# Kernel optimization log

Measured on AMD Instinct MI355X. Metric: run time of the kernel, lower is better.

## Reference

```python
import jax, jax.numpy as jnp
import numpy as np

ALPHA = 1.0  # DPMConfig.alpha
N, D, K = 4096, 256, 64


def setup_inputs() -> dict:
    key = jax.random.key(0)
    k1, k2, k3, k4 = jax.random.split(key, 4)
    x = jax.random.normal(k1, (N, D), dtype=jnp.float32)
    means = jax.random.normal(k2, (K, D), dtype=jnp.float32)
    # SPD covariances: A A^T / D + 0.5 I
    A = jax.random.normal(k3, (K, D, D), dtype=jnp.float32)
    covs = jnp.einsum('kde,kfe->kdf', A, A) / D + 0.5 * jnp.eye(D, dtype=jnp.float32)
    counts = jax.random.uniform(k4, (K,), dtype=jnp.float32, minval=1.0, maxval=200.0)
    n_points = 100000
    return {"x": x, "means": means, "covs": covs, "counts": counts, "n_points": n_points}


def reference(x, means, covs, counts, n_points):
    n, d = x.shape
    k = means.shape[0]
    # deviations from every cluster mean: [N, K, D]
    dev = x[:, None, :] - means[None, :, :]
    # batched Mahalanobis solve: covs broadcast over points
    solved = jnp.linalg.solve(covs[None], dev[..., None])[..., 0]  # [N, K, D]
    quad = jnp.sum(dev * solved, axis=-1)  # [N, K]
    # logdet with the same jitter as the original
    _, log_dets = jnp.linalg.slogdet(covs + 1e-10 * jnp.eye(d, dtype=covs.dtype))  # [K]
    log_lik = -0.5 * (d * jnp.log(2.0 * jnp.pi) + log_dets[None, :] + quad)  # [N, K]
    denom = jnp.asarray(n_points, jnp.float32) + ALPHA
    log_prior = jnp.log(counts / denom)  # [K]
    log_new = jnp.log(ALPHA / denom)
    log_probs = jnp.concatenate(
        [log_lik + log_prior[None, :], jnp.full((n, 1), log_new, dtype=x.dtype)], axis=1
    )  # [N, K+1]
    # stable normalize (max-subtract + exp + sum == softmax)
    probs = jax.nn.softmax(log_probs, axis=1)
    return probs
```

## Files before the change

### kernel.cpp

```cpp
#include <hip/hip_runtime.h>
#include <math.h>


#define DD 256
#define KC 64
#define NPTS 4096
#define NT 64
#define BB 64
#define KG 8
#define CH 4
#define NCH (DD / CH)

__global__ __launch_bounds__(512) void pivot_kernel(
    const float* __restrict__ covs, float* __restrict__ S,
    float* __restrict__ Plbuf, float* __restrict__ ldp, int bs)
{
  const int k = blockIdx.x;
  const int by = blockIdx.y;
  const int tid = threadIdx.x;
  float* Pb = Plbuf + (size_t)k * BB * BB;

  __shared__ __align__(16) float Tl[BB][BB + 4];
  __shared__ __align__(16) float pivc[2][BB];
  __shared__ __align__(16) float pivr[2][BB];

  if (by < 4) {
    if (bs == 0) return;
    const int j0p = (bs - 1) * BB;
    const int r0 = by * BB;
    const float* src = ((bs == 1) ? covs : (const float*)S) + (size_t)k * DD * DD;
    float* dst = S + (size_t)k * DD * DD;

    const int rr = tid >> 3;
    const int cc = (tid & 7) * 8;
    *reinterpret_cast<float4*>(&Tl[rr][cc]) =
        *reinterpret_cast<const float4*>(&Pb[rr * BB + cc]);
    *reinterpret_cast<float4*>(&Tl[rr][cc + 4]) =
        *reinterpret_cast<const float4*>(&Pb[rr * BB + cc + 4]);
    __syncthreads();

    const int r = r0 + rr;
    if (r0 == j0p) {
      *reinterpret_cast<float4*>(&dst[(size_t)r * DD + j0p + cc]) =
          *reinterpret_cast<const float4*>(&Tl[rr][cc]);
      *reinterpret_cast<float4*>(&dst[(size_t)r * DD + j0p + cc + 4]) =
          *reinterpret_cast<const float4*>(&Tl[rr][cc + 4]);
    } else {
      float Crow[BB];
      #pragma unroll
      for (int p = 0; p < BB; p += 4) {
        float4 cv = *reinterpret_cast<const float4*>(&src[(size_t)r * DD + j0p + p]);
        Crow[p] = cv.x; Crow[p + 1] = cv.y; Crow[p + 2] = cv.z; Crow[p + 3] = cv.w;
      }
      float acc[8] = {0.f, 0.f, 0.f, 0.f, 0.f, 0.f, 0.f, 0.f};
      #pragma unroll
      for (int p = 0; p < BB; ++p) {
        float4 t0 = *reinterpret_cast<const float4*>(&Tl[p][cc]);
        float4 t1 = *reinterpret_cast<const float4*>(&Tl[p][cc + 4]);
        acc[0] = fmaf(Crow[p], t0.x, acc[0]);
        acc[1] = fmaf(Crow[p], t0.y, acc[1]);
        acc[2] = fmaf(Crow[p], t0.z, acc[2]);
        acc[3] = fmaf(Crow[p], t0.w, acc[3]);
        acc[4] = fmaf(Crow[p], t1.x, acc[4]);
        acc[5] = fmaf(Crow[p], t1.y, acc[5]);
        acc[6] = fmaf(Crow[p], t1.z, acc[6]);
        acc[7] = fmaf(Crow[p], t1.w, acc[7]);
      }
      float4 o0 = {-acc[0], -acc[1], -acc[2], -acc[3]};
      float4 o1 = {-acc[4], -acc[5], -acc[6], -acc[7]};
      *reinterpret_cast<float4*>(&dst[(size_t)r * DD + j0p + cc]) = o0;
      *reinterpret_cast<float4*>(&dst[(size_t)r * DD + j0p + cc + 4]) = o1;
    }
    return;
  }

  if (bs == 4) return;

  const int j0 = bs * BB;
  const float* psrc = ((bs == 0) ? covs : (const float*)S) + (size_t)k * DD * DD;
  const int pr = tid >> 3;
  const int pc = (tid & 7) * 8;

  float v[8];
  {
    float4 a4 = *reinterpret_cast<const float4*>(&psrc[(size_t)(j0 + pr) * DD + j0 + pc]);
    float4 b4 = *reinterpret_cast<const float4*>(&psrc[(size_t)(j0 + pr) * DD + j0 + pc + 4]);
    v[0] = a4.x; v[1] = a4.y; v[2] = a4.z; v[3] = a4.w;
    v[4] = b4.x; v[5] = b4.y; v[6] = b4.z; v[7] = b4.w;
  }
  if (pc == 0) pivc[0][pr] = v[0];
  if (pr == 0) {
    #pragma unroll
    for (int e = 0; e < 8; ++e) pivr[0][pc + e] = v[e];
  }
  __syncthreads();

  float ld = 0.0f;
  #pragma unroll 1
  for (int p = 0; p < BB; ++p) {
    const int cur = p & 1, nxt = cur ^ 1;
    const float d = pivc[cur][p];
    const float inv_d = 1.0f / d;
    if (tid == 0) ld += logf(d);
    const float cr = pivc[cur][pr];
    float rw[8];
    *reinterpret_cast<float4*>(&rw[0]) = *reinterpret_cast<const float4*>(&pivr[cur][pc]);
    *reinterpret_cast<float4*>(&rw[4]) = *reinterpret_cast<const float4*>(&pivr[cur][pc + 4]);
    #pragma unroll
    for (int e = 0; e < 8; ++e) {
      float ge = fmaf(-inv_d * cr, rw[e], v[e]);
      if (pr == p)     ge = rw[e] * inv_d;
      if (pc + e == p) ge = (pr == p) ? -inv_d : cr * inv_d;
      v[e] = ge;
    }
    if (p < BB - 1) {
      if (pr == p + 1) {
        #pragma unroll
        for (int e = 0; e < 8; ++e) pivr[nxt][pc + e] = v[e];
      }
      if (pc <= p + 1 && p + 1 < pc + 8) pivc[nxt][pr] = v[p + 1 - pc];
    }
    __syncthreads();
  }

  float4 s0 = {v[0], v[1], v[2], v[3]};
  float4 s1 = {v[4], v[5], v[6], v[7]};
  *reinterpret_cast<float4*>(&Pb[pr * BB + pc]) = s0;
  *reinterpret_cast<float4*>(&Pb[pr * BB + pc + 4]) = s1;
  if (tid == 0) ldp[bs * KC + k] = ld;
}

__global__ __launch_bounds__(512) void update_kernel(
    const float* __restrict__ covs, float* __restrict__ S,
    const float* __restrict__ Plbuf, int bs)
{
  const int k = blockIdx.x;
  const int si = blockIdx.y;
  const int t = si + (si >= bs ? 1 : 0);
  const int c0 = t * BB;
  const int j0 = bs * BB;
  const int tid = threadIdx.x;
  const float* src = ((bs == 0) ? covs : (const float*)S) + (size_t)k * DD * DD;
  float* dst = S + (size_t)k * DD * DD;

  __shared__ __align__(16) float Pl[BB][BB + 4];
  __shared__ __align__(16) float SJ[BB][BB + 4];
  __shared__ __align__(16) float Tl[BB][BB + 4];

  const float* Pb = Plbuf + (size_t)k * BB * BB;
  #pragma unroll
  for (int q = 0; q < 8; ++q) {
    int e = q * 512 + tid;
    int r = e >> 6, c = e & 63;
    Pl[r][c] = Pb[e];
    SJ[r][c] = src[(size_t)(j0 + r) * DD + c0 + c];
  }
  __syncthreads();

  {
    const int c = tid & 63;
    const int rg = (tid >> 6) * 8;
    float tv[8];
    #pragma unroll
    for (int r = 0; r < 8; ++r) tv[r] = 0.0f;
    for (int p = 0; p < BB; p += 4) {
      float s0 = SJ[p][c], s1 = SJ[p + 1][c], s2 = SJ[p + 2][c], s3 = SJ[p + 3][c];
      #pragma unroll
      for (int r = 0; r < 8; ++r) {
        float4 pv = *reinterpret_cast<const float4*>(&Pl[rg + r][p]);
        tv[r] = fmaf(pv.x, s0, fmaf(pv.y, s1, fmaf(pv.z, s2, fmaf(pv.w, s3, tv[r]))));
      }
    }
    #pragma unroll
    for (int r = 0; r < 8; ++r) Tl[rg + r][c] = tv[r];
  }
  __syncthreads();

  const int r = tid & 255;
  const int h = (tid >> 8) * 32;
  const bool inJ = (r >= j0) && (r < j0 + BB);
  if (inJ) {
    #pragma unroll
    for (int c = 0; c < 32; c += 4) {
      float4 tv4 = *reinterpret_cast<const float4*>(&Tl[r - j0][h + c]);
      float4 o = {-tv4.x, -tv4.y, -tv4.z, -tv4.w};
      *reinterpret_cast<float4*>(&dst[(size_t)r * DD + c0 + h + c]) = o;
    }
  } else {
    float Crow[BB];
    #pragma unroll
    for (int p = 0; p < BB; p += 4) {
      float4 cv = *reinterpret_cast<const float4*>(&src[(size_t)r * DD + j0 + p]);
      Crow[p] = cv.x; Crow[p + 1] = cv.y; Crow[p + 2] = cv.z; Crow[p + 3] = cv.w;
    }
    #pragma unroll
    for (int c = 0; c < 32; c += 4) {
      float4 acc = *reinterpret_cast<const float4*>(&src[(size_t)r * DD + c0 + h + c]);
      #pragma unroll
      for (int p = 0; p < BB; ++p) {
        float4 tv4 = *reinterpret_cast<const float4*>(&Tl[p][h + c]);
        acc.x = fmaf(Crow[p], tv4.x, acc.x);
        acc.y = fmaf(Crow[p], tv4.y, acc.y);
        acc.z = fmaf(Crow[p], tv4.z, acc.z);
        acc.w = fmaf(Crow[p], tv4.w, acc.w);
      }
      *reinterpret_cast<float4*>(&dst[(size_t)r * DD + c0 + h + c]) = acc;
    }
  }
}

__global__ __launch_bounds__(256) void w_kernel(
    const float* __restrict__ S, const float* __restrict__ means,
    const float* __restrict__ counts, const int* __restrict__ n_points_p,
    const float* __restrict__ ldp, float* __restrict__ cA,
    float* __restrict__ wv)
{
  const int k = blockIdx.x;
  const int tid = threadIdx.x;
  if (tid == 0) {
    float denom = (float)(*n_points_p) + 1.0f;
    float ld = ldp[k] + ldp[KC + k] + ldp[2 * KC + k] + ldp[3 * KC + k];
    cA[k] = logf(counts[k] / denom) - 0.5f * (470.49652900079047f + ld);
  }
  const float* Sk = S + (size_t)k * DD * DD;
  __shared__ float mus[DD];
  mus[tid] = means[(size_t)k * DD + tid];
  __syncthreads();
  float a0 = 0.f, a1 = 0.f, a2 = 0.f, a3 = 0.f;
  for (int j = 0; j < DD; j += 4) {
    a0 = fmaf(Sk[(size_t)(j + 0) * DD + tid], mus[j + 0], a0);
    a1 = fmaf(Sk[(size_t)(j + 1) * DD + tid], mus[j + 1], a1);
    a2 = fmaf(Sk[(size_t)(j + 2) * DD + tid], mus[j + 2], a2);
    a3 = fmaf(Sk[(size_t)(j + 3) * DD + tid], mus[j + 3], a3);
  }
  wv[(size_t)k * DD + tid] = (a0 + a1) + (a2 + a3);
}

__global__ __launch_bounds__(256, 2) void quad_kernel(
    const float* __restrict__ X, const float* __restrict__ means,
    const float* __restrict__ S, const float* __restrict__ cA,
    const float* __restrict__ wv, float* __restrict__ lp)
{
  __shared__ __align__(16) float XT[DD][NT];
  __shared__ __align__(16) float Pl2[2][CH * DD];
  __shared__ __align__(16) float muw[2][2][DD];
  __shared__ __align__(16) float lpb[KG][NT];

  const int tid = threadIdx.x;
  const int n0 = blockIdx.x * NT;
  const int k0 = blockIdx.y * KG;

  #pragma unroll
  for (int q = 0; q < 16; ++q) {
    int f = q * 1024 + tid * 4;
    int r = f >> 8;
    int c = f & 255;
    float4 xv = *reinterpret_cast<const float4*>(X + (size_t)(n0 + r) * DD + c);
    int rs = r ^ (((c >> 2) & 15) << 2);
    XT[c + 0][rs] = xv.x;
    XT[c + 1][rs] = xv.y;
    XT[c + 2][rs] = xv.z;
    XT[c + 3][rs] = xv.w;
  }

  const int tn = tid & 7;
  const int tj = tid >> 3;

  #pragma unroll 1
  for (int kp = 0; kp < KG / 2; ++kp) {
    const int k1 = k0 + kp * 2;
    const int k2 = k1 + 1;
    const float* S1 = S + (size_t)k1 * DD * DD;
    const float* S2 = S + (size_t)k2 * DD * DD;

    __syncthreads();
    muw[0][0][tid] = means[(size_t)k1 * DD + tid];
    muw[0][1][tid] = wv[(size_t)k1 * DD + tid];
    muw[1][0][tid] = means[(size_t)k2 * DD + tid];
    muw[1][1][tid] = wv[(size_t)k2 * DD + tid];

    float4 pre0 = *reinterpret_cast<const float4*>(S1 + tid * 4);
    float4 pre1 = *reinterpret_cast<const float4*>(S2 + tid * 4);

    float y0[8][8], y1[8][8];
    #pragma unroll
    for (int a = 0; a < 8; ++a)
      #pragma unroll
      for (int b = 0; b < 8; ++b) { y0[a][b] = 0.0f; y1[a][b] = 0.0f; }

    #pragma unroll 1
    for (int ct = 0; ct < NCH; ++ct) {
      __syncthreads();
      *reinterpret_cast<float4*>(&Pl2[0][tid * 4]) = pre0;
      *reinterpret_cast<float4*>(&Pl2[1][tid * 4]) = pre1;
      if (ct < NCH - 1) {
        pre0 = *reinterpret_cast<const float4*>(S1 + (size_t)(ct + 1) * CH * DD + tid * 4);
        pre1 = *reinterpret_cast<const float4*>(S2 + (size_t)(ct + 1) * CH * DD + tid * 4);
      }
      __syncthreads();

      #pragma unroll
      for (int il = 0; il < CH; ++il) {
        const int i = ct * CH + il;
        const int sw = ((i >> 2) & 15) << 2;
        float xv[8], p0[8], p1[8];
        *reinterpret_cast<float4*>(&xv[0]) =
            *reinterpret_cast<const float4*>(&XT[i][(tn * 8) ^ sw]);
        *reinterpret_cast<float4*>(&xv[4]) =
            *reinterpret_cast<const float4*>(&XT[i][(tn * 8 + 4) ^ sw]);
        *reinterpret_cast<float4*>(&p0[0]) =
            *reinterpret_cast<const float4*>(&Pl2[0][il * DD + tj * 8]);
        *reinterpret_cast<float4*>(&p0[4]) =
            *reinterpret_cast<const float4*>(&Pl2[0][il * DD + tj * 8 + 4]);
        *reinterpret_cast<float4*>(&p1[0]) =
            *reinterpret_cast<const float4*>(&Pl2[1][il * DD + tj * 8]);
        *reinterpret_cast<float4*>(&p1[4]) =
            *reinterpret_cast<const float4*>(&Pl2[1][il * DD + tj * 8 + 4]);
        #pragma unroll
        for (int a = 0; a < 8; ++a)
          #pragma unroll
          for (int b = 0; b < 8; ++b) {
            y0[a][b] = fmaf(xv[a], p0[b], y0[a][b]);
            y1[a][b] = fmaf(xv[a], p1[b], y1[a][b]);
          }
      }
    }

    float s0[8], s1[8];
    #pragma unroll
    for (int a = 0; a < 8; ++a) { s0[a] = 0.0f; s1[a] = 0.0f; }
    #pragma unroll
    for (int b = 0; b < 8; ++b) {
      const int j = tj * 8 + b;
      const int swj = ((j >> 2) & 15) << 2;
      float dv[8];
      *reinterpret_cast<float4*>(&dv[0]) =
          *reinterpret_cast<const float4*>(&XT[j][(tn * 8) ^ swj]);
      *reinterpret_cast<float4*>(&dv[4]) =
          *reinterpret_cast<const float4*>(&XT[j][(tn * 8 + 4) ^ swj]);
      const float m1 = muw[0][0][j], w1 = muw[0][1][j];
      const float m2 = muw[1][0][j], w2 = muw[1][1][j];
      #pragma unroll
      for (int a = 0; a < 8; ++a) {
        s0[a] = fmaf(dv[a] - m1, y0[a][b] - w1, s0[a]);
        s1[a] = fmaf(dv[a] - m2, y1[a][b] - w2, s1[a]);
      }
    }

    float* qred = &Pl2[0][0];
    __syncthreads();
    #pragma unroll
    for (int a = 0; a < 8; a += 4)
      *reinterpret_cast<float4*>(&qred[tj * 64 + tn * 8 + a]) =
          *reinterpret_cast<const float4*>(&s0[a]);
    __syncthreads();
    if (tid < 64) {
      float qa = 0.f, qb = 0.f, qc = 0.f, qd = 0.f;
      #pragma unroll
      for (int t = 0; t < 32; t += 4) {
        qa += qred[(t + 0) * 64 + tid];
        qb += qred[(t + 1) * 64 + tid];
        qc += qred[(t + 2) * 64 + tid];
        qd += qred[(t + 3) * 64 + tid];
      }
      lpb[2 * kp][tid] = fmaf(0.5f, (qa + qb) + (qc + qd), cA[k1]);
    }
    __syncthreads();
    #pragma unroll
    for (int a = 0; a < 8; a += 4)
      *reinterpret_cast<float4*>(&qred[tj * 64 + tn * 8 + a]) =
          *reinterpret_cast<const float4*>(&s1[a]);
    __syncthreads();
    if (tid < 64) {
      float qa = 0.f, qb = 0.f, qc = 0.f, qd = 0.f;
      #pragma unroll
      for (int t = 0; t < 32; t += 4) {
        qa += qred[(t + 0) * 64 + tid];
        qb += qred[(t + 1) * 64 + tid];
        qc += qred[(t + 2) * 64 + tid];
        qd += qred[(t + 3) * 64 + tid];
      }
      lpb[2 * kp + 1][tid] = fmaf(0.5f, (qa + qb) + (qc + qd), cA[k2]);
    }
  }

  __syncthreads();
  if (tid < 128) {
    const int n = tid >> 1;
    const int h = (tid & 1) * 4;
    float4 o = {lpb[h + 0][n], lpb[h + 1][n], lpb[h + 2][n], lpb[h + 3][n]};
    *reinterpret_cast<float4*>(&lp[(size_t)(n0 + n) * KC + k0 + h]) = o;
  }
}

__global__ __launch_bounds__(64) void softmax_kernel(
    const float* __restrict__ lp, const int* __restrict__ n_points_p,
    float* __restrict__ out)
{
  const int n = blockIdx.x;
  const int l = threadIdx.x;
  const float denom = (float)(*n_points_p) + 1.0f;
  const float log_new = -logf(denom);

  float v = lp[(size_t)n * KC + l];
  float m = v;
  #pragma unroll
  for (int off = 32; off > 0; off >>= 1) m = fmaxf(m, __shfl_xor(m, off, 64));
  m = fmaxf(m, log_new);

  float e = expf(v - m);
  float s = e;
  #pragma unroll
  for (int off = 32; off > 0; off >>= 1) s += __shfl_xor(s, off, 64);
  float enew = expf(log_new - m);
  s += enew;

  out[(size_t)n * (KC + 1) + l] = e / s;
  if (l == 0) out[(size_t)n * (KC + 1) + KC] = enew / s;
}

extern "C" void kernel_launch(void* const* d_in, const int* in_sizes, int n_in,
                              void* d_out, int out_size, void* d_ws, size_t ws_size,
                              hipStream_t stream)
{
  const float* x       = (const float*)d_in[0];
  const float* means   = (const float*)d_in[1];
  const float* covs    = (const float*)d_in[2];
  const float* counts  = (const float*)d_in[3];
  const int*   n_points = (const int*)d_in[4];

  float* S   = (float*)d_ws;
  float* cA  = S + (size_t)KC * DD * DD;
  float* ldp = cA + KC;
  float* lp  = ldp + 4 * KC;
  float* Plbuf = lp;
  float* out = (float*)d_out;
  float* wv = out;

  for (int bs = 0; bs < 4; ++bs) {
    pivot_kernel<<<dim3(KC, 5), 512, 0, stream>>>(covs, S, Plbuf, ldp, bs);
    update_kernel<<<dim3(KC, 3), 512, 0, stream>>>(covs, S, Plbuf, bs);
  }
  pivot_kernel<<<dim3(KC, 5), 512, 0, stream>>>(covs, S, Plbuf, ldp, 4);
  w_kernel<<<KC, 256, 0, stream>>>(S, means, counts, n_points, ldp, cA, wv);
  quad_kernel<<<dim3(NPTS / NT, KC / KG), 256, 0, stream>>>(x, means, S, cA, wv, lp);
  softmax_kernel<<<NPTS, 64, 0, stream>>>(lp, n_points, out);
}
```

Measured before the change: 776.9 us.

## Process one cluster per pass in quad kernel with larger S chunks

The quad kernel now processes one cluster per iteration instead of two, which halves the per-thread accumulator registers from 128 to 64. It also doubles the chunk of S staged per sync from 4 to 8 rows, and the per-block cluster group is halved to 4, doubling the grid in y. The minimum-occupancy hint in launch bounds is dropped. The aim is lower register pressure and fewer barriers per FLOP, at the cost of re-reading the X tile into shared memory twice as often across blocks and less reuse of each XT load per FMA.

```diff
diff --git a/kernel.cpp b/kernel.cpp
--- a/kernel.cpp
+++ b/kernel.cpp
@@ -7,8 +7,8 @@
 #define NPTS 4096
 #define NT 64
 #define BB 64
-#define KG 8
-#define CH 4
+#define KG 4
+#define CH 8
 #define NCH (DD / CH)
 
 __global__ __launch_bounds__(512) void pivot_kernel(
@@ -236,14 +236,14 @@
   wv[(size_t)k * DD + tid] = (a0 + a1) + (a2 + a3);
 }
 
-__global__ __launch_bounds__(256, 2) void quad_kernel(
+__global__ __launch_bounds__(256) void quad_kernel(
     const float* __restrict__ X, const float* __restrict__ means,
     const float* __restrict__ S, const float* __restrict__ cA,
     const float* __restrict__ wv, float* __restrict__ lp)
 {
   __shared__ __align__(16) float XT[DD][NT];
-  __shared__ __align__(16) float Pl2[2][CH * DD];
-  __shared__ __align__(16) float muw[2][2][DD];
+  __shared__ __align__(16) float Pl[CH * DD];
+  __shared__ __align__(16) float muw[2][DD];
   __shared__ __align__(16) float lpb[KG][NT];
 
   const int tid = threadIdx.x;
@@ -265,37 +265,36 @@
 
   const int tn = tid & 7;
   const int tj = tid >> 3;
+  const int f0 = tid * 4;
+  const int f1 = 1024 + tid * 4;
 
   #pragma unroll 1
-  for (int kp = 0; kp < KG / 2; ++kp) {
-    const int k1 = k0 + kp * 2;
-    const int k2 = k1 + 1;
-    const float* S1 = S + (size_t)k1 * DD * DD;
-    const float* S2 = S + (size_t)k2 * DD * DD;
+  for (int kk = 0; kk < KG; ++kk) {
+    const int k = k0 + kk;
+    const float* Sk = S + (size_t)k * DD * DD;
 
     __syncthreads();
-    muw[0][0][tid] = means[(size_t)k1 * DD + tid];
-    muw[0][1][tid] = wv[(size_t)k1 * DD + tid];
-    muw[1][0][tid] = means[(size_t)k2 * DD + tid];
-    muw[1][1][tid] = wv[(size_t)k2 * DD + tid];
-
-    float4 pre0 = *reinterpret_cast<const float4*>(S1 + tid * 4);
-    float4 pre1 = *reinterpret_cast<const float4*>(S2 + tid * 4);
-
-    float y0[8][8], y1[8][8];
+    muw[0][tid] = means[(size_t)k * DD + tid];
+    muw[1][tid] = wv[(size_t)k * DD + tid];
+
+    float4 pre0 = *reinterpret_cast<const float4*>(Sk + f0);
+    float4 pre1 = *reinterpret_cast<const float4*>(Sk + f1);
+
+    float y[8][8];
     #pragma unroll
     for (int a = 0; a < 8; ++a)
       #pragma unroll
-      for (int b = 0; b < 8; ++b) { y0[a][b] = 0.0f; y1[a][b] = 0.0f; }
+      for (int b = 0; b < 8; ++b) y[a][b] = 0.0f;
 
     #pragma unroll 1
     for (int ct = 0; ct < NCH; ++ct) {
       __syncthreads();
-      *reinterpret_cast<float4*>(&Pl2[0][tid * 4]) = pre0;
-      *reinterpret_cast<float4*>(&Pl2[1][tid * 4]) = pre1;
+      *reinterpret_cast<float4*>(&Pl[f0]) = pre0;
+      *reinterpret_cast<float4*>(&Pl[f1]) = pre1;
       if (ct < NCH - 1) {
-        pre0 = *reinterpret_cast<const float4*>(S1 + (size_t)(ct + 1) * CH * DD + tid * 4);
-        pre1 = *reinterpret_cast<const float4*>(S2 + (size_t)(ct + 1) * CH * DD + tid * 4);
+        const float* srcp = Sk + (size_t)(ct + 1) * CH * DD;
+        pre0 = *reinterpret_cast<const float4*>(srcp + f0);
+        pre1 = *reinterpret_cast<const float4*>(srcp + f1);
       }
       __syncthreads();
 
@@ -303,32 +302,26 @@
       for (int il = 0; il < CH; ++il) {
         const int i = ct * CH + il;
         const int sw = ((i >> 2) & 15) << 2;
-        float xv[8], p0[8], p1[8];
+        float xv[8], pv[8];
         *reinterpret_cast<float4*>(&xv[0]) =
             *reinterpret_cast<const float4*>(&XT[i][(tn * 8) ^ sw]);
         *reinterpret_cast<float4*>(&xv[4]) =
             *reinterpret_cast<const float4*>(&XT[i][(tn * 8 + 4) ^ sw]);
-        *reinterpret_cast<float4*>(&p0[0]) =
-            *reinterpret_cast<const float4*>(&Pl2[0][il * DD + tj * 8]);
-        *reinterpret_cast<float4*>(&p0[4]) =
-            *reinterpret_cast<const float4*>(&Pl2[0][il * DD + tj * 8 + 4]);
-        *reinterpret_cast<float4*>(&p1[0]) =
-            *reinterpret_cast<const float4*>(&Pl2[1][il * DD + tj * 8]);
-        *reinterpret_cast<float4*>(&p1[4]) =
-            *reinterpret_cast<const float4*>(&Pl2[1][il * DD + tj * 8 + 4]);
+        *reinterpret_cast<float4*>(&pv[0]) =
+            *reinterpret_cast<const float4*>(&Pl[il * DD + tj * 8]);
+        *reinterpret_cast<float4*>(&pv[4]) =
+            *reinterpret_cast<const float4*>(&Pl[il * DD + tj * 8 + 4]);
         #pragma unroll
         for (int a = 0; a < 8; ++a)
           #pragma unroll
-          for (int b = 0; b < 8; ++b) {
-            y0[a][b] = fmaf(xv[a], p0[b], y0[a][b]);
-            y1[a][b] = fmaf(xv[a], p1[b], y1[a][b]);
-          }
-      }
-    }
-
-    float s0[8], s1[8];
-    #pragma unroll
-    for (int a = 0; a < 8; ++a) { s0[a] = 0.0f; s1[a] = 0.0f; }
+          for (int b = 0; b < 8; ++b)
+            y[a][b] = fmaf(xv[a], pv[b], y[a][b]);
+      }
+    }
+
+    float s[8];
+    #pragma unroll
+    for (int a = 0; a < 8; ++a) s[a] = 0.0f;
     #pragma unroll
     for (int b = 0; b < 8; ++b) {
       const int j = tj * 8 + b;
@@ -338,21 +331,19 @@
           *reinterpret_cast<const float4*>(&XT[j][(tn * 8) ^ swj]);
       *reinterpret_cast<float4*>(&dv[4]) =
           *reinterpret_cast<const float4*>(&XT[j][(tn * 8 + 4) ^ swj]);
-      const float m1 = muw[0][0][j], w1 = muw[0][1][j];
-      const float m2 = muw[1][0][j], w2 = muw[1][1][j];
-      #pragma unroll
-      for (int a = 0; a < 8; ++a) {
-        s0[a] = fmaf(dv[a] - m1, y0[a][b] - w1, s0[a]);
-        s1[a] = fmaf(dv[a] - m2, y1[a][b] - w2, s1[a]);
-      }
-    }
-
-    float* qred = &Pl2[0][0];
+      const float mj = muw[0][j];
+      const float wj = muw[1][j];
+      #pragma unroll
+      for (int a = 0; a < 8; ++a)
+        s[a] = fmaf(dv[a] - mj, y[a][b] - wj, s[a]);
+    }
+
+    float* qred = &Pl[0];
     __syncthreads();
-    #pragma unroll
-    for (int a = 0; a < 8; a += 4)
-      *reinterpret_cast<float4*>(&qred[tj * 64 + tn * 8 + a]) =
-          *reinterpret_cast<const float4*>(&s0[a]);
+    *reinterpret_cast<float4*>(&qred[tj * 64 + tn * 8]) =
+        *reinterpret_cast<const float4*>(&s[0]);
+    *reinterpret_cast<float4*>(&qred[tj * 64 + tn * 8 + 4]) =
+        *reinterpret_cast<const float4*>(&s[4]);
     __syncthreads();
     if (tid < 64) {
       float qa = 0.f, qb = 0.f, qc = 0.f, qd = 0.f;
@@ -363,33 +354,14 @@
         qc += qred[(t + 2) * 64 + tid];
         qd += qred[(t + 3) * 64 + tid];
       }
-      lpb[2 * kp][tid] = fmaf(0.5f, (qa + qb) + (qc + qd), cA[k1]);
-    }
-    __syncthreads();
-    #pragma unroll
-    for (int a = 0; a < 8; a += 4)
-      *reinterpret_cast<float4*>(&qred[tj * 64 + tn * 8 + a]) =
-          *reinterpret_cast<const float4*>(&s1[a]);
-    __syncthreads();
-    if (tid < 64) {
-      float qa = 0.f, qb = 0.f, qc = 0.f, qd = 0.f;
-      #pragma unroll
-      for (int t = 0; t < 32; t += 4) {
-        qa += qred[(t + 0) * 64 + tid];
-        qb += qred[(t + 1) * 64 + tid];
-        qc += qred[(t + 2) * 64 + tid];
-        qd += qred[(t + 3) * 64 + tid];
-      }
-      lpb[2 * kp + 1][tid] = fmaf(0.5f, (qa + qb) + (qc + qd), cA[k2]);
+      lpb[kk][tid] = fmaf(0.5f, (qa + qb) + (qc + qd), cA[k]);
     }
   }
 
   __syncthreads();
-  if (tid < 128) {
-    const int n = tid >> 1;
-    const int h = (tid & 1) * 4;
-    float4 o = {lpb[h + 0][n], lpb[h + 1][n], lpb[h + 2][n], lpb[h + 3][n]};
-    *reinterpret_cast<float4*>(&lp[(size_t)(n0 + n) * KC + k0 + h]) = o;
+  if (tid < 64) {
+    float4 o = {lpb[0][tid], lpb[1][tid], lpb[2][tid], lpb[3][tid]};
+    *reinterpret_cast<float4*>(&lp[(size_t)(n0 + tid) * KC + k0]) = o;
   }
 }
 
```

Result: faster. 648.2 us (-16.6%).
